# Optimization experiments

Measured on AMD Instinct MI355X. Metric: run time of the kernel, lower is better.

Reference implementation:

```python
import jax, jax.numpy as jnp
import numpy as np

B, N, DM, DE, H, L = 4, 256, 128, 8, 2 and 2, 8  # placeholder, real values below
B, N, DM, DE, H, L = 4, 256, 128, 8, 8, 2
D = DM // H  # per-head dim = 16
INNER = H * D


def setup_inputs() -> dict:
    key = jax.random.key(0)
    ks = jax.random.split(key, 20)
    nodes = jax.random.normal(ks[0], (B, N, DM), dtype=jnp.float32)
    edges = jax.random.normal(ks[1], (B, N, N, DE), dtype=jnp.float32)
    adjacency = (jax.random.uniform(ks[2], (B, N, N)) < 0.1).astype(jnp.float32)
    s = 0.02
    p = {
        'Wq': jax.random.normal(ks[3], (L, DM, INNER)) * s,
        'bq': jnp.zeros((L, INNER)),
        'Wk': jax.random.normal(ks[4], (L, DM, INNER)) * s,
        'bk': jnp.zeros((L, INNER)),
        'Wv': jax.random.normal(ks[5], (L, DM, INNER)) * s,
        'bv': jnp.zeros((L, INNER)),
        'We': jax.random.normal(ks[6], (L, DE, INNER)) * s,
        'be': jnp.zeros((L, INNER)),
        'Wres': jax.random.normal(ks[7], (L, DM, DM)) * s,
        'bres': jnp.zeros((L, DM)),
        'Wgate': jax.random.normal(ks[8], (L, 3 * DM, 1)) * s,
        'ln_g': jnp.ones((L, DM)),
        'ln_b': jnp.zeros((L, DM)),
    }
    return {'nodes': nodes, 'edges': edges, 'adjacency': adjacency, **p}


def _adj_softmax(sim, adj):
    # Faithful to source: torch.mean(x, dim, keepdim=True)[0] indexes batch 0,
    # giving a (N,1) shift broadcast over all batch*head rows.
    means = jnp.mean(sim, axis=-1, keepdims=True)[0]
    x_exp = jnp.exp(sim - means) * adj
    s = jnp.sum(x_exp, axis=-1, keepdims=True)
    s = jnp.where(s == 0, 1.0, s)
    return x_exp / s


def reference(nodes, edges, adjacency, Wq, bq, Wk, bk, Wv, bv, We, be,
              Wres, bres, Wgate, ln_g, ln_b):
    b, n, dm = nodes.shape
    h, d = H, DM // H
    scale = 1.0 / jnp.sqrt(jnp.float32(d))
    adj = jnp.broadcast_to(adjacency[:, None], (b, h, n, n)).reshape(b * h, n, n)
    x = nodes
    for l in range(L):  # fixed small layer count
        def heads(t):  # (b,n,h*d) -> (b*h, n, d)
            return t.reshape(b, n, h, d).transpose(0, 2, 1, 3).reshape(b * h, n, d)
        q = heads(x @ Wq[l] + bq[l])
        k = heads(x @ Wk[l] + bk[l])
        v = heads(x @ Wv[l] + bv[l])
        # edge features: (b,n,n,h,d) -> (b*h, n, n, d)
        e = (edges @ We[l] + be[l]).reshape(b, n, n, h, d)
        e = e.transpose(0, 3, 1, 2, 4).reshape(b * h, n, n, d)
        ke = k[:, None, :, :] + e
        ve = v[:, None, :, :] + e
        sim = jnp.einsum('bid,bijd->bij', q, ke) * scale
        attn = _adj_softmax(sim, adj)
        out = jnp.einsum('bij,bijd->bid', attn, ve)
        out = out.reshape(b, h, n, d).transpose(0, 2, 1, 3).reshape(b, n, h * d)
        # GatedResidual
        res = x @ Wres[l] + bres[l]
        gate_in = jnp.concatenate([out, res, out - res], axis=-1)
        g = jax.nn.sigmoid(gate_in @ Wgate[l])
        y = out * g + res * (1 - g)
        mu = jnp.mean(y, axis=-1, keepdims=True)
        var = jnp.var(y, axis=-1, keepdims=True)
        y = (y - mu) / jnp.sqrt(var + 1e-5) * ln_g[l] + ln_b[l]
        x = jax.nn.relu(y)
    return x
```

## Files before the change

kernel.cpp:

```cpp
#include <hip/hip_runtime.h>

#define BB 4
#define NN 256
#define DMM 128
#define DEE 8
#define HH 8
#define DD 16
#define LAYERS 2
#define SCALE 0.25f
#define PS 260

struct Params {
  const float *nodes, *edges, *adjacency;
  const float *Wq, *bq, *Wk, *bk, *Wv, *bv, *We, *be, *Wres, *bres, *Wgate, *lng, *lnb;
  const float *src;
  float *x, *q, *k, *v, *res;
  float *out;
  int layer;
};

__global__ __launch_bounds__(256) void k_proj(Params P){
  const int t = threadIdx.x;
  const int m = t >> 6;
  const int cp = t & 63;
  const int row0 = blockIdx.x * 4;
  const int l = P.layer;
  const float *W, *bia; float* dst;
  if (m==0){ W = P.Wq + l*DMM*DMM; bia = P.bq + l*DMM; dst = P.q; }
  else if (m==1){ W = P.Wk + l*DMM*DMM; bia = P.bk + l*DMM; dst = P.k; }
  else if (m==2){ W = P.Wv + l*DMM*DMM; bia = P.bv + l*DMM; dst = P.v; }
  else { W = P.Wres + l*DMM*DMM; bia = P.bres + l*DMM; dst = P.res; }
  const float2 bv2 = *(const float2*)(bia + 2*cp);
  float acc0[4] = {bv2.x,bv2.x,bv2.x,bv2.x};
  float acc1[4] = {bv2.y,bv2.y,bv2.y,bv2.y};
  const float2* W2 = (const float2*)W;
  const float* xr = P.src + row0*DMM;
  #pragma unroll 8
  for (int kk=0; kk<DMM; kk++){
    float2 w = W2[kk*64+cp];
    #pragma unroll
    for (int r=0;r<4;r++){
      float xv = xr[r*DMM+kk];
      acc0[r] += xv*w.x; acc1[r] += xv*w.y;
    }
  }
  #pragma unroll
  for (int r=0;r<4;r++){
    *(float2*)(dst + (row0+r)*DMM + 2*cp) = make_float2(acc0[r], acc1[r]);
  }
}

__global__ __launch_bounds__(256) void k_attn(Params P){
  const int t = threadIdx.x;
  const int b = blockIdx.x >> 8;
  const int i = blockIdx.x & 255;
  const int l = P.layer;

  __shared__ float qs[128];
  __shared__ float qwe_s[64];
  __shared__ float qbe_s[8];
  __shared__ float es[8*PS];
  __shared__ float ps[8*PS];
  __shared__ float red_s[32];
  __shared__ float ssum_s[8];
  __shared__ float g_s[64];
  __shared__ float res_s[128];
  __shared__ float red_a[2], red_b[2], red_c[2];

  if (t < 128) qs[t] = P.q[(b*NN+i)*DMM + t];
  __syncthreads();
  if (t < 64){
    const int h = t>>3, c = t&7;
    const float* Wer = P.We + l*DEE*DMM + c*DMM + h*DD;
    float a = 0.f;
    #pragma unroll
    for (int d=0; d<DD; d++) a += qs[h*DD+d]*Wer[d];
    qwe_s[t] = a;
    if (c==0){
      const float* ber = P.be + l*DMM + h*DD;
      float a2 = 0.f;
      #pragma unroll
      for (int d=0; d<DD; d++) a2 += qs[h*DD+d]*ber[d];
      qbe_s[h] = a2;
    }
  }
  __syncthreads();

  {
    const int j = t;
    const float4* er4 = (const float4*)(P.edges + ((size_t)(b*NN+i)*NN + j)*DEE);
    float4 e0 = er4[0], e1 = er4[1];
    float ec[8] = {e0.x,e0.y,e0.z,e0.w, e1.x,e1.y,e1.z,e1.w};
    #pragma unroll
    for (int c=0;c<8;c++) es[c*PS+j] = ec[c];
    const float adj = P.adjacency[(size_t)(b*NN+i)*NN + j];
    const float4* kr = (const float4*)(P.k + (b*NN+j)*DMM);
    const float* qg = P.q + (b*NN+i)*DMM;
    float preg[8];
    #pragma unroll
    for (int h=0; h<HH; h++){
      float4 k0 = kr[h*4+0], k1 = kr[h*4+1], k2 = kr[h*4+2], k3 = kr[h*4+3];
      const float* qh = qg + h*DD;
      float sim = qbe_s[h];
      sim += qh[0]*k0.x + qh[1]*k0.y + qh[2]*k0.z + qh[3]*k0.w;
      sim += qh[4]*k1.x + qh[5]*k1.y + qh[6]*k1.z + qh[7]*k1.w;
      sim += qh[8]*k2.x + qh[9]*k2.y + qh[10]*k2.z + qh[11]*k2.w;
      sim += qh[12]*k3.x + qh[13]*k3.y + qh[14]*k3.z + qh[15]*k3.w;
      const float4* qw4 = (const float4*)(qwe_s + h*8);
      float4 wA = qw4[0], wB = qw4[1];
      sim += ec[0]*wA.x + ec[1]*wA.y + ec[2]*wA.z + ec[3]*wA.w;
      sim += ec[4]*wB.x + ec[5]*wB.y + ec[6]*wB.z + ec[7]*wB.w;
      sim *= SCALE;
      float p = __expf(sim) * adj;
      preg[h] = p;
      ps[h*PS+j] = p;
    }
    #pragma unroll
    for (int h=0; h<HH; h++){
      float v = preg[h];
      #pragma unroll
      for (int off=32; off; off>>=1) v += __shfl_xor(v, off, 64);
      if ((t&63)==0) red_s[(t>>6)*8 + h] = v;
    }
  }
  __syncthreads();

  float pv = 0.f;
  if (t < 128){
    const int h = t>>4, d = t&15;
    const float* vcol = P.v + b*NN*DMM + h*DD + d;
    const float4* pr = (const float4*)(ps + h*PS);
    #pragma unroll 4
    for (int jq=0; jq<64; jq++){
      float4 pp = pr[jq];
      const float* vv = vcol + jq*4*DMM;
      pv += pp.x*vv[0] + pp.y*vv[DMM] + pp.z*vv[2*DMM] + pp.w*vv[3*DMM];
    }
  } else if (t < 192){
    const int h = (t-128)>>3, c = (t-128)&7;
    const float4* pr = (const float4*)(ps + h*PS);
    const float4* er = (const float4*)(es + c*PS);
    float g = 0.f;
    #pragma unroll 4
    for (int jq=0; jq<64; jq++){
      float4 pp = pr[jq], ee = er[jq];
      g += pp.x*ee.x + pp.y*ee.y + pp.z*ee.z + pp.w*ee.w;
    }
    g_s[h*8+c] = g;
  } else {
    const int u = t - 192;
    const float2 rv = *(const float2*)(P.res + (b*NN+i)*DMM + 2*u);
    res_s[2*u] = rv.x; res_s[2*u+1] = rv.y;
    if (t >= 248){
      const int h = t - 248;
      ssum_s[h] = red_s[h] + red_s[8+h] + red_s[16+h] + red_s[24+h];
    }
  }
  __syncthreads();

  float o = 0.f, rr = 0.f;
  if (t < 128){
    const int h = t>>4;
    const float* Wec = P.We + l*DEE*DMM + t;
    float eacc = 0.f;
    #pragma unroll
    for (int c=0;c<8;c++) eacc += Wec[c*DMM] * g_s[h*8+c];
    const float ssum = ssum_s[h];
    const float denom = (ssum==0.f) ? 1.f : ssum;
    const float bev = P.be[l*DMM + t];
    o = (pv + eacc + ssum*bev) / denom;
    rr = res_s[t];
    const float* Wg = P.Wgate + l*3*DMM;
    float contrib = o*Wg[t] + rr*Wg[DMM+t] + (o-rr)*Wg[2*DMM+t];
    #pragma unroll
    for (int off=32; off; off>>=1) contrib += __shfl_xor(contrib, off, 64);
    if ((t&63)==0) red_a[t>>6] = contrib;
  }
  __syncthreads();

  float y = 0.f;
  if (t < 128){
    const float gs = red_a[0] + red_a[1];
    const float gate = 1.f/(1.f + __expf(-gs));
    y = o*gate + rr*(1.f-gate);
    float s1 = y, s2 = y*y;
    #pragma unroll
    for (int off=32; off; off>>=1){ s1 += __shfl_xor(s1, off, 64); s2 += __shfl_xor(s2, off, 64); }
    if ((t&63)==0){ red_b[t>>6] = s1; red_c[t>>6] = s2; }
  }
  __syncthreads();

  if (t < 128){
    const float mu  = (red_b[0]+red_b[1]) * (1.f/128.f);
    const float var = (red_c[0]+red_c[1]) * (1.f/128.f) - mu*mu;
    const float inv = rsqrtf(var + 1e-5f);
    float yn = (y - mu)*inv*P.lng[l*DMM+t] + P.lnb[l*DMM+t];
    yn = fmaxf(yn, 0.f);
    if (l == LAYERS-1) P.out[(b*NN+i)*DMM + t] = yn;
    else               P.x  [(b*NN+i)*DMM + t] = yn;
  }
}

extern "C" void kernel_launch(void* const* d_in, const int* in_sizes, int n_in,
                              void* d_out, int out_size, void* d_ws, size_t ws_size,
                              hipStream_t stream) {
  Params P;
  P.nodes     = (const float*)d_in[0];
  P.edges     = (const float*)d_in[1];
  P.adjacency = (const float*)d_in[2];
  P.Wq   = (const float*)d_in[3];  P.bq   = (const float*)d_in[4];
  P.Wk   = (const float*)d_in[5];  P.bk   = (const float*)d_in[6];
  P.Wv   = (const float*)d_in[7];  P.bv   = (const float*)d_in[8];
  P.We   = (const float*)d_in[9];  P.be   = (const float*)d_in[10];
  P.Wres = (const float*)d_in[11]; P.bres = (const float*)d_in[12];
  P.Wgate= (const float*)d_in[13];
  P.lng  = (const float*)d_in[14]; P.lnb  = (const float*)d_in[15];

  float* f = (float*)d_ws;
  const int S = BB*NN*DMM;
  P.x = f; P.q = f + S; P.k = f + 2*S; P.v = f + 3*S; P.res = f + 4*S;
  P.out = (float*)d_out;

  for (int l = 0; l < LAYERS; l++){
    P.layer = l;
    P.src = (l == 0) ? P.nodes : P.x;
    k_proj <<<256,  256, 0, stream>>>(P);
    k_attn <<<BB*NN,256, 0, stream>>>(P);
  }
}
```

Before: 157.2 us.

## Fuse projection and attention for all layers into one cooperative persistent kernel

After: 450.3 us. 186% more time.

```diff
diff --git a/kernel.cpp b/kernel.cpp
--- a/kernel.cpp
+++ b/kernel.cpp
@@ -1,4 +1,6 @@
 #include <hip/hip_runtime.h>
+#include <hip/hip_cooperative_groups.h>
+namespace cg = cooperative_groups;
 
 #define BB 4
 #define NN 256
@@ -13,11 +15,205 @@
 struct Params {
   const float *nodes, *edges, *adjacency;
   const float *Wq, *bq, *Wk, *bk, *Wv, *bv, *We, *be, *Wres, *bres, *Wgate, *lng, *lnb;
+  float *kbuf, *vbuf;
   const float *src;
   float *x, *q, *k, *v, *res;
   float *out;
   int layer;
 };
+
+__global__ void k_fused2(Params P){
+  const int t = threadIdx.x;
+  const int row0 = blockIdx.x*2;
+  const int row1 = row0+1;
+  const int b = row0 >> 8;
+  cg::grid_group grid = cg::this_grid();
+
+  __shared__ float xloc[2][128];
+  __shared__ float qs[2][128];
+  __shared__ float res_s[2][128];
+  __shared__ float qwe_s[2][64];
+  __shared__ float qbe_s[2][8];
+  __shared__ float es[8*PS];
+  __shared__ float ps[8*PS];
+  __shared__ float red_s[32];
+  __shared__ float ssum_s[8];
+  __shared__ float g_s[64];
+  __shared__ float red_a[2], red_b[2], red_c[2];
+
+  if (t < 128) xloc[0][t]     = P.nodes[(size_t)row0*DMM + t];
+  else         xloc[1][t-128] = P.nodes[(size_t)row1*DMM + (t-128)];
+  float ec[2][8]; float adjv[2];
+  #pragma unroll
+  for (int r=0;r<2;r++){
+    const float4* er4 = (const float4*)(P.edges + ((size_t)(row0+r)*NN + t)*DEE);
+    float4 e0 = er4[0], e1 = er4[1];
+    ec[r][0]=e0.x; ec[r][1]=e0.y; ec[r][2]=e0.z; ec[r][3]=e0.w;
+    ec[r][4]=e1.x; ec[r][5]=e1.y; ec[r][6]=e1.z; ec[r][7]=e1.w;
+    adjv[r] = P.adjacency[(size_t)(row0+r)*NN + t];
+  }
+  __syncthreads();
+
+  for (int l=0; l<LAYERS; l++){
+    {
+      const int m = t>>6, cp = t&63;
+      const float *W, *bia;
+      if (m==0){ W=P.Wq+l*DMM*DMM;   bia=P.bq+l*DMM; }
+      else if (m==1){ W=P.Wk+l*DMM*DMM;   bia=P.bk+l*DMM; }
+      else if (m==2){ W=P.Wv+l*DMM*DMM;   bia=P.bv+l*DMM; }
+      else          { W=P.Wres+l*DMM*DMM; bia=P.bres+l*DMM; }
+      const float2 bv2 = *(const float2*)(bia+2*cp);
+      float a00=bv2.x, a01=bv2.y, a10=bv2.x, a11=bv2.y;
+      const float2* W2 = (const float2*)W;
+      #pragma unroll 8
+      for (int kk=0; kk<DMM; kk++){
+        float2 w = W2[kk*64+cp];
+        float x0 = xloc[0][kk], x1 = xloc[1][kk];
+        a00 += x0*w.x; a01 += x0*w.y;
+        a10 += x1*w.x; a11 += x1*w.y;
+      }
+      if (m==0){
+        qs[0][2*cp]=a00; qs[0][2*cp+1]=a01; qs[1][2*cp]=a10; qs[1][2*cp+1]=a11;
+      } else if (m==1){
+        *(float2*)(P.kbuf + ((size_t)l*BB*NN + row0)*DMM + 2*cp) = make_float2(a00,a01);
+        *(float2*)(P.kbuf + ((size_t)l*BB*NN + row1)*DMM + 2*cp) = make_float2(a10,a11);
+      } else if (m==2){
+        *(float2*)(P.vbuf + ((size_t)l*BB*NN + row0)*DMM + 2*cp) = make_float2(a00,a01);
+        *(float2*)(P.vbuf + ((size_t)l*BB*NN + row1)*DMM + 2*cp) = make_float2(a10,a11);
+      } else {
+        res_s[0][2*cp]=a00; res_s[0][2*cp+1]=a01; res_s[1][2*cp]=a10; res_s[1][2*cp+1]=a11;
+      }
+    }
+    __syncthreads();
+
+    if (t < 128){
+      const int r = t>>6, u = t&63, h = u>>3, c = u&7;
+      const float* Wer = P.We + l*DEE*DMM + c*DMM + h*DD;
+      float a = 0.f;
+      #pragma unroll
+      for (int d=0; d<DD; d++) a += qs[r][h*DD+d]*Wer[d];
+      qwe_s[r][u] = a;
+      if (c==0){
+        const float* ber = P.be + l*DMM + h*DD;
+        float a2=0.f;
+        #pragma unroll
+        for (int d=0; d<DD; d++) a2 += qs[r][h*DD+d]*ber[d];
+        qbe_s[r][h] = a2;
+      }
+    }
+    __threadfence();
+    grid.sync();
+    __threadfence();
+
+    for (int r=0; r<2; r++){
+      const int row = row0 + r;
+      {
+        const int j = t;
+        #pragma unroll
+        for (int c=0;c<8;c++) es[c*PS+j] = ec[r][c];
+        const float4* kr = (const float4*)(P.kbuf + ((size_t)l*BB*NN + b*NN + j)*DMM);
+        float preg[8];
+        #pragma unroll
+        for (int h=0; h<HH; h++){
+          float4 k0=kr[h*4+0], k1=kr[h*4+1], k2=kr[h*4+2], k3=kr[h*4+3];
+          const float4* q4 = (const float4*)(&qs[r][h*DD]);
+          float4 qa=q4[0], qb=q4[1], qc=q4[2], qd=q4[3];
+          float sim = qbe_s[r][h];
+          sim += qa.x*k0.x + qa.y*k0.y + qa.z*k0.z + qa.w*k0.w;
+          sim += qb.x*k1.x + qb.y*k1.y + qb.z*k1.z + qb.w*k1.w;
+          sim += qc.x*k2.x + qc.y*k2.y + qc.z*k2.z + qc.w*k2.w;
+          sim += qd.x*k3.x + qd.y*k3.y + qd.z*k3.z + qd.w*k3.w;
+          const float4* qw4 = (const float4*)(&qwe_s[r][h*8]);
+          float4 wA=qw4[0], wB=qw4[1];
+          sim += ec[r][0]*wA.x + ec[r][1]*wA.y + ec[r][2]*wA.z + ec[r][3]*wA.w;
+          sim += ec[r][4]*wB.x + ec[r][5]*wB.y + ec[r][6]*wB.z + ec[r][7]*wB.w;
+          sim *= SCALE;
+          float p = __expf(sim)*adjv[r];
+          preg[h]=p; ps[h*PS+j]=p;
+        }
+        #pragma unroll
+        for (int h=0; h<HH; h++){
+          float v = preg[h];
+          #pragma unroll
+          for (int off=32; off; off>>=1) v += __shfl_xor(v, off, 64);
+          if ((t&63)==0) red_s[(t>>6)*8+h] = v;
+        }
+      }
+      __syncthreads();
+
+      float pv = 0.f;
+      if (t < 128){
+        const int h = t>>4;
+        const float* vcol = P.vbuf + ((size_t)l*BB*NN + b*NN)*DMM + t;
+        const float4* pr = (const float4*)(ps + h*PS);
+        #pragma unroll 4
+        for (int jq=0; jq<64; jq++){
+          float4 pp = pr[jq];
+          const float* vv = vcol + jq*4*DMM;
+          pv += pp.x*vv[0] + pp.y*vv[DMM] + pp.z*vv[2*DMM] + pp.w*vv[3*DMM];
+        }
+      } else if (t < 192){
+        const int h=(t-128)>>3, c=(t-128)&7;
+        const float4* pr = (const float4*)(ps + h*PS);
+        const float4* er = (const float4*)(es + c*PS);
+        float g=0.f;
+        #pragma unroll 4
+        for (int jq=0; jq<64; jq++){
+          float4 pp=pr[jq], ee=er[jq];
+          g += pp.x*ee.x + pp.y*ee.y + pp.z*ee.z + pp.w*ee.w;
+        }
+        g_s[h*8+c]=g;
+      } else if (t >= 248){
+        const int h=t-248;
+        ssum_s[h] = red_s[h]+red_s[8+h]+red_s[16+h]+red_s[24+h];
+      }
+      __syncthreads();
+
+      float o=0.f, rr=0.f;
+      if (t<128){
+        const int h = t>>4;
+        const float* Wec = P.We + l*DEE*DMM + t;
+        float eacc=0.f;
+        #pragma unroll
+        for (int c=0;c<8;c++) eacc += Wec[c*DMM]*g_s[h*8+c];
+        const float ssum = ssum_s[h];
+        const float denom = (ssum==0.f)?1.f:ssum;
+        const float bev = P.be[l*DMM+t];
+        o = (pv + eacc + ssum*bev)/denom;
+        rr = res_s[r][t];
+        const float* Wg = P.Wgate + l*3*DMM;
+        float contrib = o*Wg[t] + rr*Wg[DMM+t] + (o-rr)*Wg[2*DMM+t];
+        #pragma unroll
+        for (int off=32; off; off>>=1) contrib += __shfl_xor(contrib, off, 64);
+        if ((t&63)==0) red_a[t>>6]=contrib;
+      }
+      __syncthreads();
+
+      float y=0.f;
+      if (t<128){
+        const float gs = red_a[0]+red_a[1];
+        const float gate = 1.f/(1.f+__expf(-gs));
+        y = o*gate + rr*(1.f-gate);
+        float s1=y, s2=y*y;
+        #pragma unroll
+        for (int off=32; off; off>>=1){ s1+=__shfl_xor(s1,off,64); s2+=__shfl_xor(s2,off,64); }
+        if ((t&63)==0){ red_b[t>>6]=s1; red_c[t>>6]=s2; }
+      }
+      __syncthreads();
+
+      if (t<128){
+        const float mu  = (red_b[0]+red_b[1])*(1.f/128.f);
+        const float var = (red_c[0]+red_c[1])*(1.f/128.f) - mu*mu;
+        const float inv = rsqrtf(var+1e-5f);
+        float yn = (y-mu)*inv*P.lng[l*DMM+t] + P.lnb[l*DMM+t];
+        yn = fmaxf(yn, 0.f);
+        if (l==LAYERS-1) P.out[(size_t)row*DMM+t] = yn;
+        else             xloc[r][t] = yn;
+      }
+      __syncthreads();
+    }
+  }
+}
 
 __global__ __launch_bounds__(256) void k_proj(Params P){
   const int t = threadIdx.x;
@@ -127,8 +323,8 @@
 
   float pv = 0.f;
   if (t < 128){
-    const int h = t>>4, d = t&15;
-    const float* vcol = P.v + b*NN*DMM + h*DD + d;
+    const int h = t>>4;
+    const float* vcol = P.v + b*NN*DMM + t;
     const float4* pr = (const float4*)(ps + h*PS);
     #pragma unroll 4
     for (int jq=0; jq<64; jq++){
@@ -218,13 +414,29 @@
 
   float* f = (float*)d_ws;
   const int S = BB*NN*DMM;
-  P.x = f; P.q = f + S; P.k = f + 2*S; P.v = f + 3*S; P.res = f + 4*S;
+  P.kbuf = f;
+  P.vbuf = f + 2*S;
+  P.x = f + 4*S; P.q = f + 5*S; P.k = f + 6*S; P.v = f + 7*S; P.res = f + 8*S;
   P.out = (float*)d_out;
+  P.layer = 0; P.src = P.nodes;
+
+  hipStreamCaptureStatus cs = hipStreamCaptureStatusNone;
+  (void)hipStreamIsCapturing(stream, &cs);
+  const bool capturing = (cs != hipStreamCaptureStatusNone);
+  static int g_coop = 0;
+  if (g_coop == 1 || (g_coop == 0 && !capturing)){
+    void* kargs[] = { (void*)&P };
+    hipError_t e = hipLaunchCooperativeKernel((void*)k_fused2, dim3(BB*NN/2), dim3(256),
+                                              kargs, 0, stream);
+    if (e == hipSuccess){ g_coop = 1; return; }
+    g_coop = -1;
+    (void)hipGetLastError();
+  }
 
   for (int l = 0; l < LAYERS; l++){
     P.layer = l;
     P.src = (l == 0) ? P.nodes : P.x;
-    k_proj <<<256,  256, 0, stream>>>(P);
-    k_attn <<<BB*NN,256, 0, stream>>>(P);
+    hipLaunchKernelGGL(k_proj, dim3(256),   dim3(256), 0, stream, P);
+    hipLaunchKernelGGL(k_attn, dim3(BB*NN), dim3(256), 0, stream, P);
   }
 }
```
